# Kernel optimization log

Hardware: AMD Instinct MI355X
Metric: run time of the kernel (lower is better)

The kernel has to match this reference:

```python
import jax, jax.numpy as jnp
from jax import lax
import numpy as np

HIDDEN = 50


def setup_inputs() -> dict:
    key = jax.random.key(0)
    ks = jax.random.split(key, 7)
    B, T, I, H, O = 2048, 512, 1, HIDDEN, 1
    s = 1.0 / np.sqrt(H)  # PyTorch nn.RNN init scale (uniform); we use normal*s for simplicity
    return {
        "x": jax.random.normal(ks[0], (B, T, I), dtype=jnp.float32),
        "W_ih": jax.random.normal(ks[1], (H, I), dtype=jnp.float32) * s,
        "W_hh": jax.random.normal(ks[2], (H, H), dtype=jnp.float32) * s,
        "b_ih": jax.random.normal(ks[3], (H,), dtype=jnp.float32) * s,
        "b_hh": jax.random.normal(ks[4], (H,), dtype=jnp.float32) * s,
        "W_fc": jax.random.normal(ks[5], (O, H), dtype=jnp.float32) * s,
        "b_fc": jax.random.normal(ks[6], (O,), dtype=jnp.float32) * s,
    }


def reference(x, W_ih, W_hh, b_ih, b_hh, W_fc, b_fc):
    # Vanilla tanh RNN (batch_first), h0 = 0; return fc(h_T).
    B = x.shape[0]
    H = W_hh.shape[0]
    # Precompute input projections for all timesteps: [T, B, H]
    xproj = jnp.einsum("bti,hi->tbh", x, W_ih) + b_ih

    def step(h, xt):
        h_new = jnp.tanh(xt + h @ W_hh.T + b_hh)
        return h_new, None

    h0 = jnp.zeros((B, H), dtype=x.dtype)
    hT, _ = lax.scan(step, h0, xproj)
    return hT @ W_fc.T + b_fc  # [B, 1]
```

## Files before the change

kernel.cpp:

```cpp
#include <hip/hip_runtime.h>

#define HID 50
#define TSTEPS 512

typedef _Float16 h2v __attribute__((ext_vector_type(2)));

__device__ __forceinline__ float fdot2(h2v a, h2v b, float c) {
#if __has_builtin(__builtin_amdgcn_fdot2)
    return __builtin_amdgcn_fdot2(a, b, c, false);
#else
    asm("v_dot2_f32_f16 %0, %1, %2, %0" : "+v"(c) : "v"(a), "v"(b));
    return c;
#endif
}

__device__ __forceinline__ h2v bits_to_h2(unsigned u) {
    h2v r; __builtin_memcpy(&r, &u, sizeof(r)); return r;
}

__global__ __launch_bounds__(64) __attribute__((amdgpu_waves_per_eu(2, 2)))
void rnn_fused(
    const float* __restrict__ x,
    const float* __restrict__ W_ih,
    const float* __restrict__ W_hh,
    const float* __restrict__ b_ih,
    const float* __restrict__ b_hh,
    const float* __restrict__ W_fc,
    const float* __restrict__ b_fc,
    float* __restrict__ out)
{
    const int b = blockIdx.x;
    const int j = threadIdx.x;
    __shared__ __align__(16) _Float16 hht[64];
    __shared__ float xbuf[64];

    const int jj = (j < HID) ? j : 0;
    const float SC = 2.8853900817779268f;

    h2v w2[25];
#pragma unroll
    for (int m = 0; m < 25; ++m) {
        h2v t;
        t.x = (_Float16)(W_hh[jj * HID + 2 * m]     * SC);
        t.y = (_Float16)(W_hh[jj * HID + 2 * m + 1] * SC);
        w2[m] = t;
    }

    const float wih  = W_ih[jj] * SC;
    const float btot = (b_ih[jj] + b_hh[jj]) * SC;
    const float wfc  = (j < HID) ? W_fc[jj] : 0.0f;
    const float bfc  = b_fc[0];

    const float* xb = x + (size_t)b * TSTEPS;
    float xv = xb[j];
    float hn = 0.0f;
    hht[j] = (_Float16)0.0f;
    __syncthreads();

    for (int c = 0; c < TSTEPS / 64; ++c) {
        xbuf[j] = xv;
        float xv_next = 0.0f;
        if (c + 1 < TSTEPS / 64) xv_next = xb[(c + 1) * 64 + j];
        __syncthreads();

        for (int g = 0; g < 8; ++g) {
#pragma unroll
            for (int ii = 0; ii < 8; ++ii) {
                const int t = g * 8 + ii;
                const float xt = xbuf[t];
                float a0 = fmaf(xt, wih, btot);
                float a1 = 0.0f, a2 = 0.0f, a3 = 0.0f;

                const uint4* h8 = reinterpret_cast<const uint4*>(hht);
#pragma unroll
                for (int q = 0; q < 7; ++q) {
                    const uint4 u = h8[q];
                    const int m = 4 * q;
                    a0 = fdot2(bits_to_h2(u.x), w2[m], a0);
                    if (m + 1 < 25) a1 = fdot2(bits_to_h2(u.y), w2[m + 1], a1);
                    if (m + 2 < 25) a2 = fdot2(bits_to_h2(u.z), w2[m + 2], a2);
                    if (m + 3 < 25) a3 = fdot2(bits_to_h2(u.w), w2[m + 3], a3);
                }
                const float z = (a0 + a1) + (a2 + a3);

                const float e = __builtin_amdgcn_exp2f(z);
                const float r = __builtin_amdgcn_rcpf(e + 1.0f);
                hn = fmaf(-2.0f, r, 1.0f);

                hht[j] = (_Float16)hn;
                __syncthreads();
            }
        }
        xv = xv_next;
    }

    float pr = hn * wfc;
#pragma unroll
    for (int off = 32; off >= 1; off >>= 1) pr += __shfl_xor(pr, off);
    if (j == 0) out[b] = pr + bfc;
}

extern "C" void kernel_launch(void* const* d_in, const int* in_sizes, int n_in,
                              void* d_out, int out_size, void* d_ws, size_t ws_size,
                              hipStream_t stream) {
    (void)d_ws; (void)ws_size; (void)n_in; (void)out_size;
    const float* x    = (const float*)d_in[0];
    const float* W_ih = (const float*)d_in[1];
    const float* W_hh = (const float*)d_in[2];
    const float* b_ih = (const float*)d_in[3];
    const float* b_hh = (const float*)d_in[4];
    const float* W_fc = (const float*)d_in[5];
    const float* b_fc = (const float*)d_in[6];
    float* out = (float*)d_out;

    const int B = in_sizes[0] / TSTEPS;
    rnn_fused<<<dim3(B), dim3(64), 0, stream>>>(x, W_ih, W_hh, b_ih, b_hh, W_fc, b_fc, out);
}
```

Measured before the change: 102.4 us.

## Interleave two batch recurrences per wave and drop per-step block barriers

Each 64-thread block now processes two batch rows. The two hidden-state recurrences are software-pipelined so that the LDS reads and writes for one row overlap the dot-product and tanh work of the other, with sched_barrier enforcing the order. Because a block is a single wavefront, the per-timestep __syncthreads calls are removed and the code relies on in-order LDS access within the wave. The grid is halved and waves_per_eu drops to 1, trading occupancy-based latency hiding for explicit interleaving inside the wave and more registers per wave.

```diff
diff --git a/kernel.cpp b/kernel.cpp
--- a/kernel.cpp
+++ b/kernel.cpp
@@ -13,12 +13,11 @@
     return c;
 #endif
 }
-
 __device__ __forceinline__ h2v bits_to_h2(unsigned u) {
     h2v r; __builtin_memcpy(&r, &u, sizeof(r)); return r;
 }
 
-__global__ __launch_bounds__(64) __attribute__((amdgpu_waves_per_eu(2, 2)))
+__global__ __launch_bounds__(64) __attribute__((amdgpu_waves_per_eu(1, 1)))
 void rnn_fused(
     const float* __restrict__ x,
     const float* __restrict__ W_ih,
@@ -29,13 +28,14 @@
     const float* __restrict__ b_fc,
     float* __restrict__ out)
 {
-    const int b = blockIdx.x;
-    const int j = threadIdx.x;
-    __shared__ __align__(16) _Float16 hht[64];
-    __shared__ float xbuf[64];
-
+    const int j  = threadIdx.x;
+    const int bA = blockIdx.x * 2;
+    const int bB = bA + 1;
     const int jj = (j < HID) ? j : 0;
     const float SC = 2.8853900817779268f;
+
+    __shared__ __align__(16) _Float16 htA[64], htB[64];
+    __shared__ float xbA[64], xbB[64];
 
     h2v w2[25];
 #pragma unroll
@@ -45,59 +45,95 @@
         t.y = (_Float16)(W_hh[jj * HID + 2 * m + 1] * SC);
         w2[m] = t;
     }
-
     const float wih  = W_ih[jj] * SC;
     const float btot = (b_ih[jj] + b_hh[jj]) * SC;
     const float wfc  = (j < HID) ? W_fc[jj] : 0.0f;
     const float bfc  = b_fc[0];
 
-    const float* xb = x + (size_t)b * TSTEPS;
-    float xv = xb[j];
-    float hn = 0.0f;
-    hht[j] = (_Float16)0.0f;
-    __syncthreads();
+    const float* xpA = x + (size_t)bA * TSTEPS;
+    const float* xpB = x + (size_t)bB * TSTEPS;
+    float xvA = xpA[j], xvB = xpB[j];
+    float hnA = 0.0f, hnB = 0.0f;
+
+    htA[j] = (_Float16)0.0f;
+    htB[j] = (_Float16)0.0f;
+    const uint4* qA = reinterpret_cast<const uint4*>(htA);
+    const uint4* qB = reinterpret_cast<const uint4*>(htB);
+    uint4 qb[7];
+#pragma unroll
+    for (int q = 0; q < 7; ++q) qb[q] = qB[q];
 
     for (int c = 0; c < TSTEPS / 64; ++c) {
-        xbuf[j] = xv;
-        float xv_next = 0.0f;
-        if (c + 1 < TSTEPS / 64) xv_next = xb[(c + 1) * 64 + j];
-        __syncthreads();
+        xbA[j] = xvA;
+        xbB[j] = xvB;
+        float xnA = 0.0f, xnB = 0.0f;
+        if (c + 1 < TSTEPS / 64) {
+            xnA = xpA[(c + 1) * 64 + j];
+            xnB = xpB[(c + 1) * 64 + j];
+        }
 
         for (int g = 0; g < 8; ++g) {
 #pragma unroll
             for (int ii = 0; ii < 8; ++ii) {
                 const int t = g * 8 + ii;
-                const float xt = xbuf[t];
-                float a0 = fmaf(xt, wih, btot);
-                float a1 = 0.0f, a2 = 0.0f, a3 = 0.0f;
 
-                const uint4* h8 = reinterpret_cast<const uint4*>(hht);
+                htA[j] = (_Float16)hnA;
+                uint4 qa[7];
 #pragma unroll
-                for (int q = 0; q < 7; ++q) {
-                    const uint4 u = h8[q];
-                    const int m = 4 * q;
-                    a0 = fdot2(bits_to_h2(u.x), w2[m], a0);
-                    if (m + 1 < 25) a1 = fdot2(bits_to_h2(u.y), w2[m + 1], a1);
-                    if (m + 2 < 25) a2 = fdot2(bits_to_h2(u.z), w2[m + 2], a2);
-                    if (m + 3 < 25) a3 = fdot2(bits_to_h2(u.w), w2[m + 3], a3);
+                for (int q = 0; q < 7; ++q) qa[q] = qA[q];
+                const float xtA = xbA[t];
+                const float xtB = xbB[t];
+                __builtin_amdgcn_sched_barrier(0);
+
+                {
+                    float a0 = fmaf(xtB, wih, btot), a1 = 0.f, a2 = 0.f, a3 = 0.f;
+#pragma unroll
+                    for (int q = 0; q < 7; ++q) {
+                        const int m = 4 * q;
+                        a0 = fdot2(bits_to_h2(qb[q].x), w2[m], a0);
+                        if (m + 1 < 25) a1 = fdot2(bits_to_h2(qb[q].y), w2[m + 1], a1);
+                        if (m + 2 < 25) a2 = fdot2(bits_to_h2(qb[q].z), w2[m + 2], a2);
+                        if (m + 3 < 25) a3 = fdot2(bits_to_h2(qb[q].w), w2[m + 3], a3);
+                    }
+                    const float z = (a0 + a1) + (a2 + a3);
+                    const float e = __builtin_amdgcn_exp2f(z);
+                    hnB = fmaf(-2.0f, __builtin_amdgcn_rcpf(e + 1.0f), 1.0f);
                 }
-                const float z = (a0 + a1) + (a2 + a3);
+                htB[j] = (_Float16)hnB;
+#pragma unroll
+                for (int q = 0; q < 7; ++q) qb[q] = qB[q];
+                __builtin_amdgcn_sched_barrier(0);
 
-                const float e = __builtin_amdgcn_exp2f(z);
-                const float r = __builtin_amdgcn_rcpf(e + 1.0f);
-                hn = fmaf(-2.0f, r, 1.0f);
-
-                hht[j] = (_Float16)hn;
-                __syncthreads();
+                {
+                    float a0 = fmaf(xtA, wih, btot), a1 = 0.f, a2 = 0.f, a3 = 0.f;
+#pragma unroll
+                    for (int q = 0; q < 7; ++q) {
+                        const int m = 4 * q;
+                        a0 = fdot2(bits_to_h2(qa[q].x), w2[m], a0);
+                        if (m + 1 < 25) a1 = fdot2(bits_to_h2(qa[q].y), w2[m + 1], a1);
+                        if (m + 2 < 25) a2 = fdot2(bits_to_h2(qa[q].z), w2[m + 2], a2);
+                        if (m + 3 < 25) a3 = fdot2(bits_to_h2(qa[q].w), w2[m + 3], a3);
+                    }
+                    const float z = (a0 + a1) + (a2 + a3);
+                    const float e = __builtin_amdgcn_exp2f(z);
+                    hnA = fmaf(-2.0f, __builtin_amdgcn_rcpf(e + 1.0f), 1.0f);
+                }
             }
         }
-        xv = xv_next;
+        xvA = xnA;
+        xvB = xnB;
     }
 
-    float pr = hn * wfc;
+    float pA = hnA * wfc, pB = hnB * wfc;
 #pragma unroll
-    for (int off = 32; off >= 1; off >>= 1) pr += __shfl_xor(pr, off);
-    if (j == 0) out[b] = pr + bfc;
+    for (int off = 32; off >= 1; off >>= 1) {
+        pA += __shfl_xor(pA, off);
+        pB += __shfl_xor(pB, off);
+    }
+    if (j == 0) {
+        out[bA] = pA + bfc;
+        out[bB] = pB + bfc;
+    }
 }
 
 extern "C" void kernel_launch(void* const* d_in, const int* in_sizes, int n_in,
@@ -114,5 +150,6 @@
     float* out = (float*)d_out;
 
     const int B = in_sizes[0] / TSTEPS;
-    rnn_fused<<<dim3(B), dim3(64), 0, stream>>>(x, W_ih, W_hh, b_ih, b_hh, W_fc, b_fc, out);
+    rnn_fused<<<dim3(B / 2), dim3(64), 0, stream>>>(x, W_ih, W_hh, b_ih, b_hh,
+                                                    W_fc, b_fc, out);
 }
```

Result: slower. 123.9 us (+21.0%).

## Split hidden rows across two waves per sequence with double-buffered hidden state

Applied to the files above, without the earlier changes.

Each block now uses two 64-lane waves, and each wave computes 25 of the 50 hidden units, so only 25 lanes per wave do useful work. The hidden state is double-buffered in shared memory so that writes for the next step do not conflict with reads of the current step. The intent is to shorten the per-step critical path or raise latency hiding by running more waves. In exchange it adds a cross-wave __syncthreads on every timestep and leaves more lanes idle. The same per-lane dot-product work is unchanged, so the gain depends on whether multi-wave barriers cost less than the extra occupancy helps.

```diff
diff --git a/kernel.cpp b/kernel.cpp
--- a/kernel.cpp
+++ b/kernel.cpp
@@ -13,12 +13,11 @@
     return c;
 #endif
 }
-
 __device__ __forceinline__ h2v bits_to_h2(unsigned u) {
     h2v r; __builtin_memcpy(&r, &u, sizeof(r)); return r;
 }
 
-__global__ __launch_bounds__(64) __attribute__((amdgpu_waves_per_eu(2, 2)))
+__global__ __launch_bounds__(128) __attribute__((amdgpu_waves_per_eu(4, 4)))
 void rnn_fused(
     const float* __restrict__ x,
     const float* __restrict__ W_ih,
@@ -29,49 +28,56 @@
     const float* __restrict__ b_fc,
     float* __restrict__ out)
 {
-    const int b = blockIdx.x;
-    const int j = threadIdx.x;
-    __shared__ __align__(16) _Float16 hht[64];
-    __shared__ float xbuf[64];
+    const int tid = threadIdx.x;
+    const int w   = tid >> 6;
+    const int l   = tid & 63;
+    const int b   = blockIdx.x;
+    const bool writer = (l < 25);
+    const int jrow = w * 25 + (writer ? l : 0);
+    const float SC = 2.8853900817779268f;
 
-    const int jj = (j < HID) ? j : 0;
-    const float SC = 2.8853900817779268f;
+    __shared__ __align__(16) _Float16 hht[2][64];
+    __shared__ __align__(16) float xbuf[64];
+    __shared__ float psum[2];
 
     h2v w2[25];
 #pragma unroll
     for (int m = 0; m < 25; ++m) {
         h2v t;
-        t.x = (_Float16)(W_hh[jj * HID + 2 * m]     * SC);
-        t.y = (_Float16)(W_hh[jj * HID + 2 * m + 1] * SC);
+        t.x = (_Float16)(W_hh[jrow * HID + 2 * m]     * SC);
+        t.y = (_Float16)(W_hh[jrow * HID + 2 * m + 1] * SC);
         w2[m] = t;
     }
-
-    const float wih  = W_ih[jj] * SC;
-    const float btot = (b_ih[jj] + b_hh[jj]) * SC;
-    const float wfc  = (j < HID) ? W_fc[jj] : 0.0f;
+    const float wih  = W_ih[jrow] * SC;
+    const float btot = (b_ih[jrow] + b_hh[jrow]) * SC;
+    const float wfc  = writer ? W_fc[jrow] : 0.0f;
     const float bfc  = b_fc[0];
 
     const float* xb = x + (size_t)b * TSTEPS;
-    float xv = xb[j];
+    float xv = 0.0f;
+    if (w == 0) xv = xb[l];
     float hn = 0.0f;
-    hht[j] = (_Float16)0.0f;
+
+    if (tid < 64) {
+        hht[0][tid] = (_Float16)0.0f;
+        hht[1][tid] = (_Float16)0.0f;
+    }
     __syncthreads();
 
     for (int c = 0; c < TSTEPS / 64; ++c) {
-        xbuf[j] = xv;
-        float xv_next = 0.0f;
-        if (c + 1 < TSTEPS / 64) xv_next = xb[(c + 1) * 64 + j];
+        if (w == 0) xbuf[l] = xv;
+        float xvn = 0.0f;
+        if (w == 0 && c + 1 < TSTEPS / 64) xvn = xb[(c + 1) * 64 + l];
         __syncthreads();
 
         for (int g = 0; g < 8; ++g) {
 #pragma unroll
             for (int ii = 0; ii < 8; ++ii) {
-                const int t = g * 8 + ii;
-                const float xt = xbuf[t];
-                float a0 = fmaf(xt, wih, btot);
-                float a1 = 0.0f, a2 = 0.0f, a3 = 0.0f;
+                const int p = ii & 1;
+                const float xt = xbuf[g * 8 + ii];
+                const uint4* h8 = reinterpret_cast<const uint4*>(&hht[p][0]);
 
-                const uint4* h8 = reinterpret_cast<const uint4*>(hht);
+                float a0 = btot, a1 = 0.f, a2 = 0.f, a3 = 0.f;
 #pragma unroll
                 for (int q = 0; q < 7; ++q) {
                     const uint4 u = h8[q];
@@ -81,23 +87,23 @@
                     if (m + 2 < 25) a2 = fdot2(bits_to_h2(u.z), w2[m + 2], a2);
                     if (m + 3 < 25) a3 = fdot2(bits_to_h2(u.w), w2[m + 3], a3);
                 }
-                const float z = (a0 + a1) + (a2 + a3);
+                const float z = fmaf(xt, wih, (a0 + a1) + (a2 + a3));
+                const float e = __builtin_amdgcn_exp2f(z);
+                hn = fmaf(-2.0f, __builtin_amdgcn_rcpf(e + 1.0f), 1.0f);
 
-                const float e = __builtin_amdgcn_exp2f(z);
-                const float r = __builtin_amdgcn_rcpf(e + 1.0f);
-                hn = fmaf(-2.0f, r, 1.0f);
-
-                hht[j] = (_Float16)hn;
+                if (writer) hht[p ^ 1][jrow] = (_Float16)hn;
                 __syncthreads();
             }
         }
-        xv = xv_next;
+        xv = xvn;
     }
 
-    float pr = hn * wfc;
+    float pr = writer ? hn * wfc : 0.0f;
 #pragma unroll
     for (int off = 32; off >= 1; off >>= 1) pr += __shfl_xor(pr, off);
-    if (j == 0) out[b] = pr + bfc;
+    if (l == 0) psum[w] = pr;
+    __syncthreads();
+    if (tid == 0) out[b] = psum[0] + psum[1] + bfc;
 }
 
 extern "C" void kernel_launch(void* const* d_in, const int* in_sizes, int n_in,
@@ -114,5 +120,6 @@
     float* out = (float*)d_out;
 
     const int B = in_sizes[0] / TSTEPS;
-    rnn_fused<<<dim3(B), dim3(64), 0, stream>>>(x, W_ih, W_hh, b_ih, b_hh, W_fc, b_fc, out);
+    rnn_fused<<<dim3(B), dim3(128), 0, stream>>>(x, W_ih, W_hh, b_ih, b_hh,
+                                                 W_fc, b_fc, out);
 }
```

Measured after the change: 189.5 us. 1.85x slower.
